# Kernel tuning notes

Measured on AMD Instinct MI355X. Metric: run time of the kernel, lower is better.

## Reference

```python
import jax, jax.numpy as jnp
import numpy as np
import math

H = 1024      # hidden_size
NH = 16       # num_heads
HD = H // NH  # head_dim
MS = 256      # memory_size
MD = 512      # memory_dim
B, S = 2, 2048


def setup_inputs() -> dict:
    key = jax.random.key(0)
    ks = jax.random.split(key, 12)
    sd = 1.0 / math.sqrt(H)
    inp = {
        "hidden_states": jax.random.normal(ks[0], (B, S, H), dtype=jnp.float32),
        "attention_mask": jnp.zeros((B, S), dtype=jnp.float32),
        "Wq": jax.random.normal(ks[1], (H, H), dtype=jnp.float32) * sd,
        "bq": jnp.zeros((H,), dtype=jnp.float32),
        "Wk": jax.random.normal(ks[2], (H, H), dtype=jnp.float32) * sd,
        "bk": jnp.zeros((H,), dtype=jnp.float32),
        "Wv": jax.random.normal(ks[3], (H, H), dtype=jnp.float32) * sd,
        "bv": jnp.zeros((H,), dtype=jnp.float32),
        "Wo": jax.random.normal(ks[4], (H, H), dtype=jnp.float32) * sd,
        "bo": jnp.zeros((H,), dtype=jnp.float32),
        "memory_values": jax.random.normal(ks[5], (MS, MD), dtype=jnp.float32),
        "Wmp": jax.random.normal(ks[6], (H, MD), dtype=jnp.float32) * (1.0 / math.sqrt(MD)),
        "bmp": jnp.zeros((H,), dtype=jnp.float32),
        "Wma": jax.random.normal(ks[7], (MS, H), dtype=jnp.float32) * sd,
        "bma": jnp.zeros((MS,), dtype=jnp.float32),
    }
    return inp


def reference(hidden_states, attention_mask, Wq, bq, Wk, bk, Wv, bv, Wo, bo,
              memory_values, Wmp, bmp, Wma, bma):
    b, s, h = hidden_states.shape
    scale = math.sqrt(HD)
    # projections (nn.Linear: x @ W.T + b)
    q = hidden_states @ Wq.T + bq
    k = hidden_states @ Wk.T + bk
    v = hidden_states @ Wv.T + bv
    # [b, nh, s, hd]
    q = q.reshape(b, s, NH, HD).transpose(0, 2, 1, 3)
    k = k.reshape(b, s, NH, HD).transpose(0, 2, 1, 3)
    v = v.reshape(b, s, NH, HD).transpose(0, 2, 1, 3)
    # full score matrix [b, nh, s, s] (faithful to original naive MHA)
    attn_scores = jnp.einsum('bhqd,bhkd->bhqk', q, k) / scale
    attn_scores = attn_scores + attention_mask[:, None, None, :] * (-1e9)
    attn_probs = jax.nn.softmax(attn_scores, axis=-1)  # dropout = identity (eval)
    attn_output = jnp.einsum('bhqk,bhkd->bhqd', attn_probs, v)
    attn_output = attn_output.transpose(0, 2, 1, 3).reshape(b, s, h)
    # memory-bank cross attention
    mem_scores = hidden_states @ Wma.T + bma            # [b, s, MS]
    mem_probs = jax.nn.softmax(mem_scores, axis=-1)
    mem_out = mem_probs @ memory_values                  # [b, s, MD]
    mem_out = mem_out @ Wmp.T + bmp                      # [b, s, H]
    combined = attn_output + 0.3 * mem_out
    return combined @ Wo.T + bo
```

## Files before the change

kernel.cpp:

```cpp
#include <hip/hip_runtime.h>

typedef __bf16 bf16;
typedef __bf16 bf16x8 __attribute__((ext_vector_type(8)));
typedef __bf16 bf16x4 __attribute__((ext_vector_type(4)));
typedef float  f32x4  __attribute__((ext_vector_type(4)));
typedef float  f32x16 __attribute__((ext_vector_type(16)));
typedef unsigned u32x2 __attribute__((ext_vector_type(2)));
typedef unsigned u32x4 __attribute__((ext_vector_type(4)));
typedef unsigned long long uptr;

#define MFMA16(a, b, c) __builtin_amdgcn_mfma_f32_16x16x32_bf16((a), (b), (c), 0, 0, 0)
#define MFMA32(a, b, c) __builtin_amdgcn_mfma_f32_32x32x16_bf16((a), (b), (c), 0, 0, 0)

__device__ __forceinline__ void gl_lds16(const void* g, void* l) {
  __builtin_amdgcn_global_load_lds(
      (__attribute__((address_space(1))) void*)(uptr)(g),
      (__attribute__((address_space(3))) void*)(uptr)(l),
      16, 0, 0);
}
__device__ __forceinline__ void gl_lds4(const void* g, void* l) {
  __builtin_amdgcn_global_load_lds(
      (__attribute__((address_space(1))) void*)(uptr)(g),
      (__attribute__((address_space(3))) void*)(uptr)(l),
      4, 0, 0);
}
__device__ __forceinline__ unsigned cvtpk_bf16(float lo, float hi) {
  unsigned r;
  asm("v_cvt_pk_bf16_f32 %0, %1, %2" : "=v"(r) : "v"(lo), "v"(hi));
  return r;
}

__global__ __launch_bounds__(256) void fused_prep(
    const float* __restrict__ X, const float* __restrict__ Wq,
    const float* __restrict__ Wk, const float* __restrict__ Wv,
    const float* __restrict__ Wo, const float* __restrict__ Wma,
    const float* __restrict__ Wmp, const float* __restrict__ mask,
    const float* __restrict__ bq, const float* __restrict__ bk,
    const float* __restrict__ bv, const float* __restrict__ mv,
    bf16* __restrict__ Xb, bf16* __restrict__ Wqkvb, bf16* __restrict__ Wob,
    bf16* __restrict__ Wmab, bf16* __restrict__ Wmpb,
    float* __restrict__ M2, float* __restrict__ bqkv, bf16* __restrict__ mvTb) {
  const int bid = blockIdx.x, t = threadIdx.x;
  const float QS = 0.125f * 1.44269504f;
  auto cvt = [&](const float* src, bf16* dst, int blk, float sc) {
    const long i = ((long)blk * 256 + t) * 4;
    const float4 v = *(const float4*)(src + i);
    bf16x4 o = {(bf16)(v.x * sc), (bf16)(v.y * sc), (bf16)(v.z * sc), (bf16)(v.w * sc)};
    *(bf16x4*)(dst + i) = o;
  };
  if (bid < 4096) cvt(X, Xb, bid, 1.0f);
  else if (bid < 5120) cvt(Wq, Wqkvb, bid - 4096, QS);
  else if (bid < 6144) cvt(Wk, Wqkvb + 1024 * 1024, bid - 5120, 1.0f);
  else if (bid < 7168) cvt(Wv, Wqkvb + 2 * 1024 * 1024, bid - 6144, 1.0f);
  else if (bid < 8192) cvt(Wo, Wob, bid - 7168, 1.0f);
  else if (bid < 8448) cvt(Wma, Wmab, bid - 8192, 1.0f);
  else if (bid < 8960) cvt(Wmp, Wmpb, bid - 8448, 1.0f);
  else if (bid < 8964) {
    const long i = ((long)(bid - 8960) * 256 + t) * 4;
    const float4 v = *(const float4*)(mask + i);
    float4 o = {v.x * -1.44269504e9f, v.y * -1.44269504e9f,
                v.z * -1.44269504e9f, v.w * -1.44269504e9f};
    *(float4*)(M2 + i) = o;
  } else if (bid < 8967) {
    const int s = bid - 8964;
    const float* src = s == 0 ? bq : (s == 1 ? bk : bv);
    const float sc = s == 0 ? QS : 1.0f;
    float4 v = *(const float4*)(src + t * 4);
    float4 o = {v.x * sc, v.y * sc, v.z * sc, v.w * sc};
    *(float4*)(bqkv + s * 1024 + t * 4) = o;
  } else {
    const int d = bid - 8967;
    mvTb[(long)d * 256 + t] = (bf16)mv[(long)t * 512 + d];
  }
}

__global__ __launch_bounds__(256) void softmax_rows256(const float* __restrict__ in,
                                                       bf16* __restrict__ out) {
  const int w = threadIdx.x >> 6, l = threadIdx.x & 63;
  const long row = (long)blockIdx.x * 4 + w;
  const float4 v = *(const float4*)(in + row * 256 + l * 4);
  float mx = fmaxf(fmaxf(v.x, v.y), fmaxf(v.z, v.w));
  mx = fmaxf(mx, __shfl_xor(mx, 1, 64));
  mx = fmaxf(mx, __shfl_xor(mx, 2, 64));
  mx = fmaxf(mx, __shfl_xor(mx, 4, 64));
  mx = fmaxf(mx, __shfl_xor(mx, 8, 64));
  mx = fmaxf(mx, __shfl_xor(mx, 16, 64));
  mx = fmaxf(mx, __shfl_xor(mx, 32, 64));
  const float e0 = __expf(v.x - mx), e1 = __expf(v.y - mx);
  const float e2 = __expf(v.z - mx), e3 = __expf(v.w - mx);
  float sm = e0 + e1 + e2 + e3;
  sm += __shfl_xor(sm, 1, 64);
  sm += __shfl_xor(sm, 2, 64);
  sm += __shfl_xor(sm, 4, 64);
  sm += __shfl_xor(sm, 8, 64);
  sm += __shfl_xor(sm, 16, 64);
  sm += __shfl_xor(sm, 32, 64);
  const float inv = 1.0f / sm;
  bf16x4 o = {(bf16)(e0 * inv), (bf16)(e1 * inv), (bf16)(e2 * inv), (bf16)(e3 * inv)};
  *(bf16x4*)(out + row * 256 + l * 4) = o;
}

template <typename OutT, bool HAS_ADD>
__global__ __launch_bounds__(256, 3) void gemm_bt(
    const bf16* __restrict__ A, const bf16* __restrict__ B,
    const float* __restrict__ bias, const bf16* __restrict__ addsrc,
    OutT* __restrict__ C, int M, int N, int K, float alpha) {
  __shared__ bf16 lA[2][128 * 64];
  __shared__ bf16 lB[2][64 * 64];
  const int tid = threadIdx.x;
  const int w = tid >> 6, l = tid & 63;
  const int hi = l >> 4, lo = l & 15;
  const int m0 = blockIdx.y * 128, n0 = blockIdx.x * 64;
  const int wm = w * 32;

  const int sr8 = l >> 3;
  const int sc = (l & 7) * 8;
  const long aRow = (long)(m0 + wm + sr8);
  const long bRow = (long)(n0 + w * 16 + sr8);

  auto stage = [&](int p, int k0) {
#pragma unroll
    for (int j = 0; j < 4; ++j)
      gl_lds16(A + (aRow + 8 * j) * K + k0 + sc, (char*)lA[p] + (wm + 8 * j) * 128);
#pragma unroll
    for (int j = 0; j < 2; ++j)
      gl_lds16(B + (bRow + 8 * j) * K + k0 + sc, (char*)lB[p] + (w * 16 + 8 * j) * 128);
  };

  f32x4 acc[2][4] = {};
  stage(0, 0);
  __syncthreads();
  const int nt = K >> 6;

  for (int t = 0; t < nt; ++t) {
    const int p = t & 1;
    if (t + 1 < nt) stage(p ^ 1, (t + 1) << 6);
#pragma unroll
    for (int kk = 0; kk < 2; ++kk) {
      bf16x8 af[2], bfr[4];
#pragma unroll
      for (int mi = 0; mi < 2; ++mi)
        af[mi] = *(const bf16x8*)((const char*)lA[p] + (wm + mi * 16 + lo) * 128 + kk * 64 + hi * 16);
#pragma unroll
      for (int ni = 0; ni < 4; ++ni)
        bfr[ni] = *(const bf16x8*)((const char*)lB[p] + (ni * 16 + lo) * 128 + kk * 64 + hi * 16);
      __builtin_amdgcn_s_setprio(1);
#pragma unroll
      for (int mi = 0; mi < 2; ++mi)
#pragma unroll
        for (int ni = 0; ni < 4; ++ni)
          acc[mi][ni] = MFMA16(af[mi], bfr[ni], acc[mi][ni]);
      __builtin_amdgcn_s_setprio(0);
    }
    __syncthreads();
  }

#pragma unroll
  for (int ni = 0; ni < 4; ++ni) {
    const int col = n0 + ni * 16 + lo;
    const float bv = bias ? bias[col] : 0.0f;
#pragma unroll
    for (int mi = 0; mi < 2; ++mi) {
      const int mrow = m0 + wm + mi * 16 + hi * 4;
#pragma unroll
      for (int r = 0; r < 4; ++r) {
        const long row = mrow + r;
        float v = (acc[mi][ni][r] + bv) * alpha;
        if (HAS_ADD) v += (float)addsrc[row * N + col];
        C[row * (long)N + col] = (OutT)v;
      }
    }
  }
}

__global__ __launch_bounds__(256, 3) void gemm_qkv(
    const bf16* __restrict__ A, const bf16* __restrict__ B,
    const float* __restrict__ bias, bf16* __restrict__ Qo,
    bf16* __restrict__ Ko, bf16* __restrict__ Vto) {
  const int K = 1024;
  __shared__ bf16 smem[2][128 * 64];
  bf16* lA = smem[0];
  bf16* lB = smem[1];
  const int tid = threadIdx.x;
  const int w = tid >> 6, l = tid & 63;
  const int hi = l >> 4, lo = l & 15;
  const int m0 = blockIdx.y * 128, n0 = blockIdx.x * 128;
  const int wm = (w >> 1) * 64, wn = (w & 1) * 64;

  const int sr = w * 32 + (l >> 3);
  const int sc = (l & 7) * 8;
  const long aBase = (long)(m0 + sr) * K + sc;
  const long bBase = (long)(n0 + sr) * K + sc;

  f32x4 acc[4][4] = {};

  for (int k0 = 0; k0 < K; k0 += 64) {
#pragma unroll
    for (int j = 0; j < 4; ++j) {
      gl_lds16(A + aBase + (long)8 * j * K + k0, (char*)lA + (w * 32 + 8 * j) * 128);
      gl_lds16(B + bBase + (long)8 * j * K + k0, (char*)lB + (w * 32 + 8 * j) * 128);
    }
    __syncthreads();
#pragma unroll
    for (int kk = 0; kk < 2; ++kk) {
      bf16x8 af[4], bfr[4];
#pragma unroll
      for (int i = 0; i < 4; ++i) {
        af[i]  = *(const bf16x8*)((const char*)lA + (wm + i * 16 + lo) * 128 + kk * 64 + hi * 16);
        bfr[i] = *(const bf16x8*)((const char*)lB + (wn + i * 16 + lo) * 128 + kk * 64 + hi * 16);
      }
#pragma unroll
      for (int mi = 0; mi < 4; ++mi)
#pragma unroll
        for (int ni = 0; ni < 4; ++ni)
          acc[mi][ni] = MFMA16(af[mi], bfr[ni], acc[mi][ni]);
    }
    __syncthreads();
  }

  const int region = n0 >> 10;
  if (region < 2) {
#pragma unroll
    for (int ni = 0; ni < 4; ++ni) {
      const int col = n0 + wn + ni * 16 + lo;
      const float bv = bias[col];
#pragma unroll
      for (int mi = 0; mi < 4; ++mi) {
        const int mrow = m0 + wm + mi * 16 + hi * 4;
#pragma unroll
        for (int r = 0; r < 4; ++r) {
          const long row = mrow + r;
          const float v = acc[mi][ni][r] + bv;
          if (region == 0) Qo[row * 1024 + col] = (bf16)v;
          else             Ko[row * 1024 + (col - 1024)] = (bf16)v;
        }
      }
    }
  } else {
    bf16* sT = smem[0];
#pragma unroll
    for (int ni = 0; ni < 4; ++ni) {
      const int cT = wn + ni * 16 + lo;
      const float bv = bias[n0 + cT];
#pragma unroll
      for (int mi = 0; mi < 4; ++mi) {
        const int rT = wm + mi * 16 + hi * 4;
        u32x2 pw = {cvtpk_bf16(acc[mi][ni][0] + bv, acc[mi][ni][1] + bv),
                    cvtpk_bf16(acc[mi][ni][2] + bv, acc[mi][ni][3] + bv)};
        *(u32x2*)((char*)sT + cT * 256 + ((rT * 2) ^ ((cT & 15) << 3))) = pw;
      }
    }
    __syncthreads();
    const long vrow0 = (long)(m0 >> 11) * 1024 + (n0 - 2048);
    const int srow = m0 & 2047;
#pragma unroll
    for (int dd = 0; dd < 32; ++dd) {
      const int d = w * 32 + dd;
      const unsigned pv = *(const unsigned*)((const char*)sT + d * 256 + ((l * 4) ^ ((d & 15) << 3)));
      *(unsigned*)((char*)(Vto + (vrow0 + d) * 2048 + srow) + l * 4) = pv;
    }
  }
}

__global__ __launch_bounds__(256, 4) void attn_fwd(
    const bf16* __restrict__ Q, const bf16* __restrict__ Km,
    const bf16* __restrict__ Vt, const float* __restrict__ M2,
    bf16* __restrict__ Opart, float* __restrict__ ml) {
  __shared__ bf16 lK[2][64 * 64];
  __shared__ bf16 lV[2][64 * 64];
  __shared__ alignas(16) float lM[2][64];
  const int tid = threadIdx.x, w = tid >> 6, l = tid & 63;
  const int q31 = l & 31, h32 = l >> 5;
  const int b = blockIdx.z >> 1, half = blockIdx.z & 1;
  const int hh = blockIdx.y, q0 = blockIdx.x * 128;
  const long S = 2048, H = 1024;
  const int kbase = half * 1024;

  bf16x8 qf[4];
  const long qrow = (long)b * S + q0 + w * 32 + q31;
#pragma unroll
  for (int sl = 0; sl < 4; ++sl)
    qf[sl] = *(const bf16x8*)(Q + qrow * H + hh * 64 + sl * 16 + h32 * 8);

  f32x16 o0 = {}, o1 = {};
  float mrun = -1e30f, lrun = 0.0f;

  const int swr = w * 16 + (l >> 3);
  const int swc = ((l & 7) ^ (l >> 3)) * 8;

  auto stage = [&](int p, int k0) {
#pragma unroll
    for (int j = 0; j < 2; ++j) {
      gl_lds16(Km + ((long)b * S + k0 + swr + 8 * j) * H + hh * 64 + swc,
               (char*)lK[p] + (w * 16 + 8 * j) * 128);
      gl_lds16(Vt + ((long)b * H + hh * 64 + swr + 8 * j) * S + k0 + swc,
               (char*)lV[p] + (w * 16 + 8 * j) * 128);
    }
    if (w == 0) gl_lds4(M2 + (long)b * S + k0 + l, (char*)lM[p]);
  };

  stage(0, kbase);
  __syncthreads();

  for (int t = 0; t < 16; ++t) {
    const int p = t & 1;
    if (t < 15) stage(p ^ 1, kbase + (t + 1) * 64);

    f32x16 s0, s1;
#pragma unroll
    for (int g = 0; g < 4; ++g) {
      const f32x4 m0 = *(const f32x4*)&lM[p][8 * g + 4 * h32];
      const f32x4 m1 = *(const f32x4*)&lM[p][32 + 8 * g + 4 * h32];
#pragma unroll
      for (int r = 0; r < 4; ++r) {
        s0[4 * g + r] = m0[r];
        s1[4 * g + r] = m1[r];
      }
    }

    __builtin_amdgcn_s_setprio(1);
#pragma unroll
    for (int sl = 0; sl < 4; ++sl) {
      const int ch = sl * 2 + h32;
      const int cx = (ch ^ (q31 & 7)) * 16;
      const bf16x8 k0f = *(const bf16x8*)((const char*)lK[p] + q31 * 128 + cx);
      const bf16x8 k1f = *(const bf16x8*)((const char*)lK[p] + (32 + q31) * 128 + cx);
      s0 = MFMA32(k0f, qf[sl], s0);
      s1 = MFMA32(k1f, qf[sl], s1);
    }
    __builtin_amdgcn_s_setprio(0);

    float mm = -1e30f;
#pragma unroll
    for (int i = 0; i < 16; ++i)
      asm("v_max3_f32 %0, %1, %2, %3" : "=v"(mm) : "v"(mm), "v"(s0[i]), "v"(s1[i]));
    float mx = fmaxf(mm, __shfl_xor(mm, 32, 64));

    if (__any(mx > mrun + 8.0f)) {
      const float mn = fmaxf(mrun, mx);
      const float f = __builtin_amdgcn_exp2f(mrun - mn);
      mrun = mn;
      lrun *= f;
      float fb[16];
#pragma unroll
      for (int reg = 0; reg < 16; ++reg)
        fb[reg] = __shfl(f, (reg & 3) + 8 * (reg >> 2) + 4 * h32, 64);
#pragma unroll
      for (int reg = 0; reg < 16; ++reg) { o0[reg] *= fb[reg]; o1[reg] *= fb[reg]; }
    }

#pragma unroll
    for (int i = 0; i < 16; ++i) s0[i] = __builtin_amdgcn_exp2f(s0[i] - mrun);
#pragma unroll
    for (int i = 0; i < 16; ++i) s1[i] = __builtin_amdgcn_exp2f(s1[i] - mrun);

    f32x16 ts;
#pragma unroll
    for (int i = 0; i < 16; ++i) ts[i] = s0[i] + s1[i];
#pragma unroll
    for (int i = 0; i < 8; ++i) ts[i] += ts[i + 8];
#pragma unroll
    for (int i = 0; i < 4; ++i) ts[i] += ts[i + 4];
    float rs = (ts[0] + ts[1]) + (ts[2] + ts[3]);
    rs += __shfl_xor(rs, 32, 64);
    lrun += rs;

    bf16x8 pa[4];
#pragma unroll
    for (int ks = 0; ks < 4; ++ks) {
      const int rb = (ks & 1) * 8;
      unsigned a0, a1, b0, b1;
      if (ks < 2) {
        a0 = cvtpk_bf16(s0[rb + 0], s0[rb + 1]);
        a1 = cvtpk_bf16(s0[rb + 2], s0[rb + 3]);
        b0 = cvtpk_bf16(s0[rb + 4], s0[rb + 5]);
        b1 = cvtpk_bf16(s0[rb + 6], s0[rb + 7]);
      } else {
        a0 = cvtpk_bf16(s1[rb + 0], s1[rb + 1]);
        a1 = cvtpk_bf16(s1[rb + 2], s1[rb + 3]);
        b0 = cvtpk_bf16(s1[rb + 4], s1[rb + 5]);
        b1 = cvtpk_bf16(s1[rb + 6], s1[rb + 7]);
      }
      const u32x2 r02 = __builtin_amdgcn_permlane32_swap(a0, b0, false, false);
      const u32x2 r13 = __builtin_amdgcn_permlane32_swap(a1, b1, false, false);
      const u32x4 pw = {r02[0], r13[0], r02[1], r13[1]};
      pa[ks] = __builtin_bit_cast(bf16x8, pw);
    }

    __builtin_amdgcn_s_setprio(1);
#pragma unroll
    for (int ks = 0; ks < 4; ++ks) {
      const int ch = ks * 2 + h32;
      const int cx = (ch ^ (q31 & 7)) * 16;
      const bf16x8 v0 = *(const bf16x8*)((const char*)lV[p] + q31 * 128 + cx);
      const bf16x8 v1 = *(const bf16x8*)((const char*)lV[p] + (32 + q31) * 128 + cx);
      o0 = MFMA32(pa[ks], v0, o0);
      o1 = MFMA32(pa[ks], v1, o1);
    }
    __builtin_amdgcn_s_setprio(0);
    __syncthreads();
  }

  if (h32 == 0) {
    float2 v = {mrun, lrun};
    ((float2*)ml)[((long)half * 4096 + (long)b * 2048 + q0 + w * 32 + q31) * 16 + hh] = v;
  }
#pragma unroll
  for (int reg = 0; reg < 16; ++reg) {
    const int row = (reg & 3) + 8 * (reg >> 2) + 4 * h32;
    const long qg = (long)b * 2048 + q0 + w * 32 + row;
    Opart[((long)half * 4096 + qg) * 1024 + hh * 64 + q31]      = (bf16)o0[reg];
    Opart[((long)half * 4096 + qg) * 1024 + hh * 64 + 32 + q31] = (bf16)o1[reg];
  }
}

__global__ __launch_bounds__(256) void attn_combine(
    const bf16* __restrict__ Opart, const float* __restrict__ ml,
    bf16* __restrict__ AO) {
  const long i = ((long)blockIdx.x * 256 + threadIdx.x) * 4;
  const long qg = i >> 10;
  const int h = (int)((i & 1023) >> 6);
  const float2 a = ((const float2*)ml)[qg * 16 + h];
  const float2 c = ((const float2*)ml)[(4096 + qg) * 16 + h];
  const float m = fmaxf(a.x, c.x);
  const float w0 = __builtin_amdgcn_exp2f(a.x - m);
  const float w1 = __builtin_amdgcn_exp2f(c.x - m);
  const float inv = 1.0f / (w0 * a.y + w1 * c.y);
  const bf16x4 O0 = *(const bf16x4*)(Opart + i);
  const bf16x4 O1 = *(const bf16x4*)(Opart + 4096L * 1024 + i);
  bf16x4 o;
#pragma unroll
  for (int j = 0; j < 4; ++j)
    o[j] = (bf16)(((float)O0[j] * w0 + (float)O1[j] * w1) * inv);
  *(bf16x4*)(AO + i) = o;
}

extern "C" void kernel_launch(void* const* d_in, const int* in_sizes, int n_in,
                              void* d_out, int out_size, void* d_ws, size_t ws_size,
                              hipStream_t stream) {
  const float* X    = (const float*)d_in[0];
  const float* mask = (const float*)d_in[1];
  const float* Wq   = (const float*)d_in[2];  const float* bq  = (const float*)d_in[3];
  const float* Wk   = (const float*)d_in[4];  const float* bk  = (const float*)d_in[5];
  const float* Wv   = (const float*)d_in[6];  const float* bv  = (const float*)d_in[7];
  const float* Wo   = (const float*)d_in[8];  const float* bo  = (const float*)d_in[9];
  const float* mv   = (const float*)d_in[10];
  const float* Wmp  = (const float*)d_in[11]; const float* bmp = (const float*)d_in[12];
  const float* Wma  = (const float*)d_in[13]; const float* bma = (const float*)d_in[14];

  char* ws = (char*)d_ws;
  size_t off = 0;
  auto alloc = [&](size_t bytes) -> void* {
    void* p = ws + off;
    off += (bytes + 255) & ~(size_t)255;
    return p;
  };
  const long MS_ = 4096;
  bf16* Xb    = (bf16*)alloc(MS_ * 1024 * 2);
  bf16* Wqkvb = (bf16*)alloc(3072L * 1024 * 2);
  bf16* Wob   = (bf16*)alloc(1024 * 1024 * 2);
  bf16* Wmab  = (bf16*)alloc(256 * 1024 * 2);
  bf16* Wmpb  = (bf16*)alloc(1024 * 512 * 2);
  bf16* mvTb  = (bf16*)alloc(512 * 256 * 2);
  float* M2   = (float*)alloc(MS_ * 4);
  float* bqkv = (float*)alloc(3072 * 4);
  bf16* Qb    = (bf16*)alloc(MS_ * 1024 * 2);
  bf16* Kb    = (bf16*)alloc(MS_ * 1024 * 2);
  bf16* Vtb   = (bf16*)alloc(MS_ * 1024 * 2);
  bf16* AO    = (bf16*)alloc(MS_ * 1024 * 2);
  char* region = (char*)alloc(2 * MS_ * 1024 * 2 + MS_ * 16 * 8 + 1024);
  bf16* Opart = (bf16*)region;
  float* ml   = (float*)(region + 2 * MS_ * 1024 * 2);
  float* MSc  = (float*)region;
  bf16* MP    = (bf16*)(region + MS_ * 256 * 4);
  bf16* MO    = Kb;
  bf16* CB    = Qb;

  fused_prep<<<9479, 256, 0, stream>>>(X, Wq, Wk, Wv, Wo, Wma, Wmp, mask,
                                       bq, bk, bv, mv,
                                       Xb, Wqkvb, Wob, Wmab, Wmpb, M2, bqkv, mvTb);
  gemm_qkv<<<dim3(24, 32), 256, 0, stream>>>(Xb, Wqkvb, bqkv, Qb, Kb, Vtb);
  attn_fwd<<<dim3(16, 16, 4), 256, 0, stream>>>(Qb, Kb, Vtb, M2, Opart, ml);
  attn_combine<<<4096, 256, 0, stream>>>(Opart, ml, AO);
  gemm_bt<float, false><<<dim3(4, 32), 256, 0, stream>>>(Xb, Wmab, bma, nullptr, MSc, 4096, 256, 1024, 1.0f);
  softmax_rows256<<<1024, 256, 0, stream>>>(MSc, MP);
  gemm_bt<bf16, false><<<dim3(8, 32), 256, 0, stream>>>(MP, mvTb, nullptr, nullptr, MO, 4096, 512, 256, 1.0f);
  gemm_bt<bf16, true><<<dim3(16, 32), 256, 0, stream>>>(MO, Wmpb, bmp, AO, CB, 4096, 1024, 512, 0.3f);
  gemm_bt<float, false><<<dim3(16, 32), 256, 0, stream>>>(CB, Wob, bo, nullptr, (float*)d_out, 4096, 1024, 1024, 1.0f);
}
```

Baseline: 153.2 us.

## Fold memory projection into output GEMM via concatenated weights and K-concat

Precomputes Wo·Wmp (scaled by 0.3) as extra columns of a concatenated weight matrix, and writes attention output and memory output side by side into a 1536-wide activation buffer. A single K=1536 output GEMM then replaces the separate Wmp projection GEMM (with its add-epilogue) and the Wo GEMM, and the bias becomes bo + 0.3·Wo·bmp. It also remaps the attention grid to a 1D launch with a swizzled block-to-tile order. The cost is a small weight-side GEMM, a naive bias matvec in the prep kernel, and different bf16 rounding from fusing the two weight matrices.

```diff
diff --git a/kernel.cpp b/kernel.cpp
--- a/kernel.cpp
+++ b/kernel.cpp
@@ -37,9 +37,11 @@
     const float* __restrict__ Wmp, const float* __restrict__ mask,
     const float* __restrict__ bq, const float* __restrict__ bk,
     const float* __restrict__ bv, const float* __restrict__ mv,
-    bf16* __restrict__ Xb, bf16* __restrict__ Wqkvb, bf16* __restrict__ Wob,
-    bf16* __restrict__ Wmab, bf16* __restrict__ Wmpb,
-    float* __restrict__ M2, float* __restrict__ bqkv, bf16* __restrict__ mvTb) {
+    const float* __restrict__ bo, const float* __restrict__ bmp,
+    bf16* __restrict__ Xb, bf16* __restrict__ Wqkvb, bf16* __restrict__ WCAT,
+    bf16* __restrict__ Wmab, bf16* __restrict__ WmpT,
+    float* __restrict__ M2, float* __restrict__ bqkv, bf16* __restrict__ mvTb,
+    float* __restrict__ bmix) {
   const int bid = blockIdx.x, t = threadIdx.x;
   const float QS = 0.125f * 1.44269504f;
   auto cvt = [&](const float* src, bf16* dst, int blk, float sc) {
@@ -52,10 +54,21 @@
   else if (bid < 5120) cvt(Wq, Wqkvb, bid - 4096, QS);
   else if (bid < 6144) cvt(Wk, Wqkvb + 1024 * 1024, bid - 5120, 1.0f);
   else if (bid < 7168) cvt(Wv, Wqkvb + 2 * 1024 * 1024, bid - 6144, 1.0f);
-  else if (bid < 8192) cvt(Wo, Wob, bid - 7168, 1.0f);
-  else if (bid < 8448) cvt(Wma, Wmab, bid - 8192, 1.0f);
-  else if (bid < 8960) cvt(Wmp, Wmpb, bid - 8448, 1.0f);
-  else if (bid < 8964) {
+  else if (bid < 8192) {
+    const long i = ((long)(bid - 7168) * 256 + t) * 4;
+    const long row = i >> 10, col = i & 1023;
+    const float4 v = *(const float4*)(Wo + i);
+    bf16x4 o = {(bf16)v.x, (bf16)v.y, (bf16)v.z, (bf16)v.w};
+    *(bf16x4*)(WCAT + row * 1536 + col) = o;
+  } else if (bid < 8448) cvt(Wma, Wmab, bid - 8192, 1.0f);
+  else if (bid < 8960) {
+    const int m = bid - 8448;
+#pragma unroll
+    for (int j = 0; j < 4; ++j) {
+      const int k = t * 4 + j;
+      WmpT[(long)m * 1024 + k] = (bf16)Wmp[(long)k * 512 + m];
+    }
+  } else if (bid < 8964) {
     const long i = ((long)(bid - 8960) * 256 + t) * 4;
     const float4 v = *(const float4*)(mask + i);
     float4 o = {v.x * -1.44269504e9f, v.y * -1.44269504e9f,
@@ -68,9 +81,18 @@
     float4 v = *(const float4*)(src + t * 4);
     float4 o = {v.x * sc, v.y * sc, v.z * sc, v.w * sc};
     *(float4*)(bqkv + s * 1024 + t * 4) = o;
-  } else {
+  } else if (bid < 9479) {
     const int d = bid - 8967;
     mvTb[(long)d * 256 + t] = (bf16)mv[(long)t * 512 + d];
+  } else {
+    const int n = (bid - 9479) * 256 + t;
+    float acc = 0.0f;
+    for (int k4 = 0; k4 < 256; ++k4) {
+      const float4 wv = *(const float4*)(Wo + (long)n * 1024 + k4 * 4);
+      const float4 bb = *(const float4*)(bmp + k4 * 4);
+      acc += wv.x * bb.x + wv.y * bb.y + wv.z * bb.z + wv.w * bb.w;
+    }
+    bmix[n] = bo[n] + 0.3f * acc;
   }
 }
 
@@ -100,11 +122,11 @@
   *(bf16x4*)(out + row * 256 + l * 4) = o;
 }
 
-template <typename OutT, bool HAS_ADD>
+template <typename OutT>
 __global__ __launch_bounds__(256, 3) void gemm_bt(
     const bf16* __restrict__ A, const bf16* __restrict__ B,
-    const float* __restrict__ bias, const bf16* __restrict__ addsrc,
-    OutT* __restrict__ C, int M, int N, int K, float alpha) {
+    const float* __restrict__ bias, OutT* __restrict__ C,
+    int M, int N, int K, int lda, int ldc, float alpha) {
   __shared__ bf16 lA[2][128 * 64];
   __shared__ bf16 lB[2][64 * 64];
   const int tid = threadIdx.x;
@@ -121,7 +143,7 @@
   auto stage = [&](int p, int k0) {
 #pragma unroll
     for (int j = 0; j < 4; ++j)
-      gl_lds16(A + (aRow + 8 * j) * K + k0 + sc, (char*)lA[p] + (wm + 8 * j) * 128);
+      gl_lds16(A + (aRow + 8 * j) * lda + k0 + sc, (char*)lA[p] + (wm + 8 * j) * 128);
 #pragma unroll
     for (int j = 0; j < 2; ++j)
       gl_lds16(B + (bRow + 8 * j) * K + k0 + sc, (char*)lB[p] + (w * 16 + 8 * j) * 128);
@@ -165,9 +187,7 @@
 #pragma unroll
       for (int r = 0; r < 4; ++r) {
         const long row = mrow + r;
-        float v = (acc[mi][ni][r] + bv) * alpha;
-        if (HAS_ADD) v += (float)addsrc[row * N + col];
-        C[row * (long)N + col] = (OutT)v;
+        C[row * (long)ldc + col] = (OutT)((acc[mi][ni][r] + bv) * alpha);
       }
     }
   }
@@ -269,12 +289,14 @@
   __shared__ bf16 lK[2][64 * 64];
   __shared__ bf16 lV[2][64 * 64];
   __shared__ alignas(16) float lM[2][64];
+  const int lin = blockIdx.x;
+  const int role = ((lin & 7) << 7) | (lin >> 3);
+  const int qt = role & 15, hh = (role >> 4) & 15, zz = role >> 8;
+  const int b = zz >> 1, half = zz & 1;
+  const int q0 = qt * 128, kbase = half * 1024;
   const int tid = threadIdx.x, w = tid >> 6, l = tid & 63;
   const int q31 = l & 31, h32 = l >> 5;
-  const int b = blockIdx.z >> 1, half = blockIdx.z & 1;
-  const int hh = blockIdx.y, q0 = blockIdx.x * 128;
   const long S = 2048, H = 1024;
-  const int kbase = half * 1024;
 
   bf16x8 qf[4];
   const long qrow = (long)b * S + q0 + w * 32 + q31;
@@ -416,7 +438,7 @@
 
 __global__ __launch_bounds__(256) void attn_combine(
     const bf16* __restrict__ Opart, const float* __restrict__ ml,
-    bf16* __restrict__ AO) {
+    bf16* __restrict__ CAT) {
   const long i = ((long)blockIdx.x * 256 + threadIdx.x) * 4;
   const long qg = i >> 10;
   const int h = (int)((i & 1023) >> 6);
@@ -428,11 +450,12 @@
   const float inv = 1.0f / (w0 * a.y + w1 * c.y);
   const bf16x4 O0 = *(const bf16x4*)(Opart + i);
   const bf16x4 O1 = *(const bf16x4*)(Opart + 4096L * 1024 + i);
+  const long row = i >> 10, col = i & 1023;
   bf16x4 o;
 #pragma unroll
   for (int j = 0; j < 4; ++j)
     o[j] = (bf16)(((float)O0[j] * w0 + (float)O1[j] * w1) * inv);
-  *(bf16x4*)(AO + i) = o;
+  *(bf16x4*)(CAT + row * 1536 + col) = o;
 }
 
 extern "C" void kernel_launch(void* const* d_in, const int* in_sizes, int n_in,
@@ -458,33 +481,36 @@
   const long MS_ = 4096;
   bf16* Xb    = (bf16*)alloc(MS_ * 1024 * 2);
   bf16* Wqkvb = (bf16*)alloc(3072L * 1024 * 2);
-  bf16* Wob   = (bf16*)alloc(1024 * 1024 * 2);
+  bf16* WCAT  = (bf16*)alloc(1024L * 1536 * 2);
   bf16* Wmab  = (bf16*)alloc(256 * 1024 * 2);
-  bf16* Wmpb  = (bf16*)alloc(1024 * 512 * 2);
+  bf16* WmpT  = (bf16*)alloc(512L * 1024 * 2);
   bf16* mvTb  = (bf16*)alloc(512 * 256 * 2);
   float* M2   = (float*)alloc(MS_ * 4);
   float* bqkv = (float*)alloc(3072 * 4);
+  float* bmix = (float*)alloc(1024 * 4);
   bf16* Qb    = (bf16*)alloc(MS_ * 1024 * 2);
   bf16* Kb    = (bf16*)alloc(MS_ * 1024 * 2);
   bf16* Vtb   = (bf16*)alloc(MS_ * 1024 * 2);
-  bf16* AO    = (bf16*)alloc(MS_ * 1024 * 2);
+  bf16* CAT   = (bf16*)alloc(MS_ * 1536 * 2);
   char* region = (char*)alloc(2 * MS_ * 1024 * 2 + MS_ * 16 * 8 + 1024);
   bf16* Opart = (bf16*)region;
   float* ml   = (float*)(region + 2 * MS_ * 1024 * 2);
   float* MSc  = (float*)region;
   bf16* MP    = (bf16*)(region + MS_ * 256 * 4);
-  bf16* MO    = Kb;
-  bf16* CB    = Qb;
-
-  fused_prep<<<9479, 256, 0, stream>>>(X, Wq, Wk, Wv, Wo, Wma, Wmp, mask,
-                                       bq, bk, bv, mv,
-                                       Xb, Wqkvb, Wob, Wmab, Wmpb, M2, bqkv, mvTb);
+
+  fused_prep<<<9483, 256, 0, stream>>>(X, Wq, Wk, Wv, Wo, Wma, Wmp, mask,
+                                       bq, bk, bv, mv, bo, bmp,
+                                       Xb, Wqkvb, WCAT, Wmab, WmpT, M2, bqkv, mvTb, bmix);
+  gemm_bt<bf16><<<dim3(8, 8), 256, 0, stream>>>(WCAT, WmpT, nullptr, WCAT + 1024,
+                                                1024, 512, 1024, 1536, 1536, 0.3f);
   gemm_qkv<<<dim3(24, 32), 256, 0, stream>>>(Xb, Wqkvb, bqkv, Qb, Kb, Vtb);
-  attn_fwd<<<dim3(16, 16, 4), 256, 0, stream>>>(Qb, Kb, Vtb, M2, Opart, ml);
-  attn_combine<<<4096, 256, 0, stream>>>(Opart, ml, AO);
-  gemm_bt<float, false><<<dim3(4, 32), 256, 0, stream>>>(Xb, Wmab, bma, nullptr, MSc, 4096, 256, 1024, 1.0f);
+  attn_fwd<<<1024, 256, 0, stream>>>(Qb, Kb, Vtb, M2, Opart, ml);
+  attn_combine<<<4096, 256, 0, stream>>>(Opart, ml, CAT);
+  gemm_bt<float><<<dim3(4, 32), 256, 0, stream>>>(Xb, Wmab, bma, MSc,
+                                                  4096, 256, 1024, 1024, 256, 1.0f);
   softmax_rows256<<<1024, 256, 0, stream>>>(MSc, MP);
-  gemm_bt<bf16, false><<<dim3(8, 32), 256, 0, stream>>>(MP, mvTb, nullptr, nullptr, MO, 4096, 512, 256, 1.0f);
-  gemm_bt<bf16, true><<<dim3(16, 32), 256, 0, stream>>>(MO, Wmpb, bmp, AO, CB, 4096, 1024, 512, 0.3f);
-  gemm_bt<float, false><<<dim3(16, 32), 256, 0, stream>>>(CB, Wob, bo, nullptr, (float*)d_out, 4096, 1024, 1024, 1.0f);
-}
+  gemm_bt<bf16><<<dim3(8, 32), 256, 0, stream>>>(MP, mvTb, nullptr, CAT + 1024,
+                                                 4096, 512, 256, 256, 1536, 1.0f);
+  gemm_bt<float><<<dim3(16, 32), 256, 0, stream>>>(CAT, WCAT, bmix, (float*)d_out,
+                                                   4096, 1024, 1536, 1536, 1024, 1.0f);
+}
```

Result: slower. 189.0 us (+23.4%).
